# Kernel optimization log

Hardware: AMD Instinct MI355X
Metric: run time of the kernel (lower is better)

The kernel has to match this reference:

```python
import math
import jax, jax.numpy as jnp
import numpy as np

B, S, E, H, DK, L, NB, V, FF, C = 4, 2048, 512, 8, 64, 2, 4, 32000, 2048, 4


def _pos_encoding(seq_len, embed_dim):
    pos = np.arange(seq_len, dtype=np.float32)[:, None]
    div = np.exp(np.arange(0, embed_dim, 2, dtype=np.float32) * (-math.log(10000.0) / embed_dim))
    pe = np.zeros((seq_len, embed_dim), dtype=np.float32)
    pe[:, 0::2] = np.sin(pos * div)
    pe[:, 1::2] = np.cos(pos * div)
    return jnp.asarray(pe)


def _layernorm(x, g, b, eps=1e-5):
    m = jnp.mean(x, axis=-1, keepdims=True)
    v = jnp.mean((x - m) ** 2, axis=-1, keepdims=True)
    return (x - m) * jax.lax.rsqrt(v + eps) * g + b


def setup_inputs() -> dict:
    key = jax.random.key(0)
    ks = jax.random.split(key, 32)
    sd = 0.02
    inp = {
        "tokens": jax.random.randint(ks[0], (B, S), 0, V, dtype=jnp.int32),
        "emb": jax.random.normal(ks[1], (V, E), jnp.float32) * sd,
        # per-block stacked params (leading dim NB)
        "Wq": jax.random.normal(ks[2], (NB, E, E), jnp.float32) * sd,
        "Wk": jax.random.normal(ks[3], (NB, E, E), jnp.float32) * sd,
        "Wv": jax.random.normal(ks[4], (NB, E, E), jnp.float32) * sd,
        "Wo": jax.random.normal(ks[5], (NB, E, E), jnp.float32) * sd,
        # quantum per-head linear stacks: [NB, L, H, DK, DK] weights, [NB, L, H, DK] biases
        "qh_w": jax.random.normal(ks[6], (NB, L, H, DK, DK), jnp.float32) * 0.1,
        "qh_b": jax.random.normal(ks[7], (NB, L, H, DK), jnp.float32) * 0.01,
        "kh_w": jax.random.normal(ks[8], (NB, L, H, DK, DK), jnp.float32) * 0.1,
        "kh_b": jax.random.normal(ks[9], (NB, L, H, DK), jnp.float32) * 0.01,
        "vh_w": jax.random.normal(ks[10], (NB, L, H, DK, DK), jnp.float32) * 0.1,
        "vh_b": jax.random.normal(ks[11], (NB, L, H, DK), jnp.float32) * 0.01,
        "ln1_g": jnp.ones((NB, E), jnp.float32),
        "ln1_b": jnp.zeros((NB, E), jnp.float32),
        "ln2_g": jnp.ones((NB, E), jnp.float32),
        "ln2_b": jnp.zeros((NB, E), jnp.float32),
        "f_w1": jax.random.normal(ks[12], (NB, E, FF), jnp.float32) * sd,
        "f_b1": jnp.zeros((NB, FF), jnp.float32),
        "f_w2": jax.random.normal(ks[13], (NB, FF, E), jnp.float32) * sd,
        "f_b2": jnp.zeros((NB, E), jnp.float32),
        "cls_w": jax.random.normal(ks[14], (E, C), jnp.float32) * sd,
        "cls_b": jnp.zeros((C,), jnp.float32),
    }
    return inp


def _quantum_apply(h, w_stack, b_stack):
    # h: [B,H,S,DK]; w_stack: [L,H,DK,DK]; b_stack: [L,H,DK]
    for l in range(L):
        h = jnp.einsum("bhsd,hde->bhse", h, w_stack[l]) + b_stack[l][None, :, None, :]
    return h


def _block(x, Wq, Wk, Wv, Wo, qh_w, qh_b, kh_w, kh_b, vh_w, vh_b,
           ln1_g, ln1_b, ln2_g, ln2_b, f_w1, f_b1, f_w2, f_b2):
    b, s, _ = x.shape
    q = (x @ Wq).reshape(b, s, H, DK).transpose(0, 2, 1, 3)  # [B,H,S,DK]
    k = (x @ Wk).reshape(b, s, H, DK).transpose(0, 2, 1, 3)
    v = (x @ Wv).reshape(b, s, H, DK).transpose(0, 2, 1, 3)
    q = _quantum_apply(q, qh_w, qh_b)
    k = _quantum_apply(k, kh_w, kh_b)
    v = _quantum_apply(v, vh_w, vh_b)
    scores = jnp.einsum("bhqd,bhkd->bhqk", q, k) / math.sqrt(DK)
    attn = jax.nn.softmax(scores, axis=-1)
    out = jnp.einsum("bhqk,bhkd->bhqd", attn, v)
    out = out.transpose(0, 2, 1, 3).reshape(b, s, E) @ Wo
    x = _layernorm(x + out, ln1_g, ln1_b)
    ffn = jax.nn.relu(x @ f_w1 + f_b1) @ f_w2 + f_b2
    return _layernorm(x + ffn, ln2_g, ln2_b)


def reference(tokens, emb, Wq, Wk, Wv, Wo, qh_w, qh_b, kh_w, kh_b, vh_w, vh_b,
              ln1_g, ln1_b, ln2_g, ln2_b, f_w1, f_b1, f_w2, f_b2, cls_w, cls_b):
    x = emb[tokens]  # [B,S,E]
    x = x + _pos_encoding(S, E)[None]
    for i in range(NB):
        x = _block(x, Wq[i], Wk[i], Wv[i], Wo[i],
                   qh_w[i], qh_b[i], kh_w[i], kh_b[i], vh_w[i], vh_b[i],
                   ln1_g[i], ln1_b[i], ln2_g[i], ln2_b[i],
                   f_w1[i], f_b1[i], f_w2[i], f_b2[i])
    x = x.mean(axis=1)  # [B,E]
    return x @ cls_w + cls_b  # [B,C]
```

## Files before the change

### kernel.cpp

```cpp
#include <hip/hip_runtime.h>
#include <hip/hip_bf16.h>
#include <math.h>

#define BB 4
#define SS 2048
#define EE 512
#define HH 8
#define DKK 64
#define LL 2
#define NBB 4
#define FFF 2048
#define CC 4
#define NBSE ((size_t)BB * SS * EE)

typedef __attribute__((ext_vector_type(8))) short bf16x8;
typedef __attribute__((ext_vector_type(4))) float f32x4;
using bf16 = __hip_bfloat16;

__device__ __forceinline__ float fast_exp2(float x) { return __builtin_amdgcn_exp2f(x); }

__device__ __forceinline__ void gload16(const bf16* g, bf16* l) {
    __builtin_amdgcn_global_load_lds((const __attribute__((address_space(1))) void*)g,
                                     (__attribute__((address_space(3))) void*)l, 16, 0, 0);
}
__device__ __forceinline__ unsigned short bf16bits(float f) {
    bf16 h = __float2bfloat16(f);
    return *(unsigned short*)&h;
}

__global__ __launch_bounds__(256) void embed_kernel(const int* __restrict__ tokens,
                                                    const float* __restrict__ emb,
                                                    float* __restrict__ x,
                                                    bf16* __restrict__ xb) {
    int i = blockIdx.x * blockDim.x + threadIdx.x;
    int total = BB * SS * EE / 2;
    if (i >= total) return;
    int pi  = i & (EE / 2 - 1);
    int row = i >> 8;
    int s   = row & (SS - 1);
    int tok = tokens[row];
    int e0  = pi * 2;
    const float kln = 9.210340371976184f / (float)EE;
    float arg = (float)s * expf(-(float)e0 * kln);
    float2 ev = *(const float2*)(emb + (size_t)tok * EE + e0);
    float2 o;
    o.x = ev.x + sinf(arg);
    o.y = ev.y + cosf(arg);
    *(float2*)(x + (size_t)row * EE + e0) = o;
    xb[(size_t)row * EE + e0]     = __float2bfloat16(o.x);
    xb[(size_t)row * EE + e0 + 1] = __float2bfloat16(o.y);
}

__global__ __launch_bounds__(256) void transpose_to_bf16(const float* __restrict__ in,
                                                         bf16* __restrict__ out,
                                                         int K, int N,
                                                         size_t zstride, int row_off) {
    const float* src = in + (size_t)blockIdx.z * K * N;
    bf16* dst = out + (size_t)blockIdx.z * zstride;
    int r0 = blockIdx.y * 64, c0 = blockIdx.x * 64;
    __shared__ float tl[64][65];
    int t = threadIdx.x;
    int lr = t >> 4, lc = (t & 15) * 4;
#pragma unroll
    for (int i = 0; i < 4; i++) {
        float4 v = *(const float4*)(src + (size_t)(r0 + lr + i * 16) * N + c0 + lc);
        tl[lr + i * 16][lc + 0] = v.x;
        tl[lr + i * 16][lc + 1] = v.y;
        tl[lr + i * 16][lc + 2] = v.z;
        tl[lr + i * 16][lc + 3] = v.w;
    }
    __syncthreads();
#pragma unroll
    for (int i = 0; i < 4; i++) {
        int n = lr + i * 16;
#pragma unroll
        for (int j = 0; j < 4; j++)
            dst[(size_t)(row_off + c0 + n) * K + r0 + lc + j] = __float2bfloat16(tl[lc + j][n]);
    }
}

#define GF_RELU 1
#define GF_SCATTER3 2
#define GF_OUTBF16 4
__global__ __launch_bounds__(256) void gemm_bf16(const bf16* __restrict__ A,
                                                 const bf16* __restrict__ BT,
                                                 const float* __restrict__ bias,
                                                 void* __restrict__ C,
                                                 int M, int N, int K, int flags) {
    __shared__ __align__(16) bf16 Asm[128 * 32];
    __shared__ __align__(16) bf16 Bsm[128 * 32];
    int t = threadIdx.x;
    int l = t & 63, w = t >> 6;
    int nbx = gridDim.x;
    int lin = blockIdx.y * nbx + blockIdx.x;
    int cpx = (nbx * gridDim.y) >> 3;
    int swz = (lin & 7) * cpx + (lin >> 3);
    int bm = (swz / nbx) * 128, bn = (swz % nbx) * 128;
    int wr = (w >> 1) * 64, wc = (w & 1) * 64;
    int lr = l & 15, lg = l >> 4;
    int ca = w * 2;
    int sr = l >> 2, sk = (l & 3) * 8;
    const bf16* ga  = A  + (size_t)(bm + ca * 16 + sr) * K + sk;
    const bf16* ga2 = ga + (size_t)16 * K;
    const bf16* gb  = BT + (size_t)(bn + ca * 16 + sr) * K + sk;
    const bf16* gb2 = gb + (size_t)16 * K;

    f32x4 acc[4][4];
#pragma unroll
    for (int m = 0; m < 4; m++)
#pragma unroll
        for (int n = 0; n < 4; n++) acc[m][n] = (f32x4){0.f, 0.f, 0.f, 0.f};

    for (int k0 = 0; k0 < K; k0 += 32) {
        __syncthreads();
        gload16(ga + k0,  &Asm[ca * 512]);
        gload16(ga2 + k0, &Asm[ca * 512 + 512]);
        gload16(gb + k0,  &Bsm[ca * 512]);
        gload16(gb2 + k0, &Bsm[ca * 512 + 512]);
        __syncthreads();
        bf16x8 af[4], bfr[4];
#pragma unroll
        for (int m = 0; m < 4; m++)
            af[m] = *(const bf16x8*)&Asm[(wr + m * 16 + lr) * 32 + lg * 8];
#pragma unroll
        for (int n = 0; n < 4; n++)
            bfr[n] = *(const bf16x8*)&Bsm[(wc + n * 16 + lr) * 32 + lg * 8];
#pragma unroll
        for (int m = 0; m < 4; m++)
#pragma unroll
            for (int n = 0; n < 4; n++)
                acc[m][n] = __builtin_amdgcn_mfma_f32_16x16x32_bf16(af[m], bfr[n], acc[m][n], 0, 0, 0);
    }

#pragma unroll
    for (int m = 0; m < 4; m++) {
        int row = bm + wr + m * 16 + lg * 4;
#pragma unroll
        for (int n = 0; n < 4; n++) {
            int col = bn + wc + n * 16 + lr;
            float bv = bias ? bias[col] : 0.f;
#pragma unroll
            for (int r = 0; r < 4; r++) {
                float v = acc[m][n][r] + bv;
                if (flags & GF_RELU) v = fmaxf(v, 0.f);
                int rr = row + r;
                if (flags & GF_SCATTER3) {
                    int tsel = col >> 9;
                    int b = rr >> 11, s = rr & (SS - 1);
                    int h = (col >> 6) & 7, dk = col & 63;
                    ((bf16*)C)[tsel * NBSE + (((size_t)(b * HH + h) * SS + s) << 6) + dk] = __float2bfloat16(v);
                } else if (flags & GF_OUTBF16) {
                    ((bf16*)C)[(size_t)rr * N + col] = __float2bfloat16(v);
                } else {
                    ((float*)C)[(size_t)rr * N + col] = v;
                }
            }
        }
    }
}

__global__ __launch_bounds__(256) void gemm_bf16_m64(const bf16* __restrict__ A,
                                                     const bf16* __restrict__ BT,
                                                     const float* __restrict__ bias,
                                                     void* __restrict__ C,
                                                     int M, int N, int K, int flags) {
    __shared__ __align__(16) bf16 Asm[64 * 32];
    __shared__ __align__(16) bf16 Bsm[128 * 32];
    int t = threadIdx.x;
    int l = t & 63, w = t >> 6;
    int nbx = gridDim.x;
    int lin = blockIdx.y * nbx + blockIdx.x;
    int cpx = (nbx * gridDim.y) >> 3;
    int swz = (lin & 7) * cpx + (lin >> 3);
    int bm = (swz / nbx) * 64, bn = (swz % nbx) * 128;
    int wr = (w >> 1) * 32, wc = (w & 1) * 64;
    int lr = l & 15, lg = l >> 4;
    int ca = w * 2;
    int sr = l >> 2, sk = (l & 3) * 8;
    const bf16* ga  = A  + (size_t)(bm + w * 16 + sr) * K + sk;
    const bf16* gb  = BT + (size_t)(bn + ca * 16 + sr) * K + sk;
    const bf16* gb2 = gb + (size_t)16 * K;

    f32x4 acc[2][4];
#pragma unroll
    for (int m = 0; m < 2; m++)
#pragma unroll
        for (int n = 0; n < 4; n++) acc[m][n] = (f32x4){0.f, 0.f, 0.f, 0.f};

    for (int k0 = 0; k0 < K; k0 += 32) {
        __syncthreads();
        gload16(ga + k0,  &Asm[w * 512]);
        gload16(gb + k0,  &Bsm[ca * 512]);
        gload16(gb2 + k0, &Bsm[ca * 512 + 512]);
        __syncthreads();
        bf16x8 af[2], bfr[4];
#pragma unroll
        for (int m = 0; m < 2; m++)
            af[m] = *(const bf16x8*)&Asm[(wr + m * 16 + lr) * 32 + lg * 8];
#pragma unroll
        for (int n = 0; n < 4; n++)
            bfr[n] = *(const bf16x8*)&Bsm[(wc + n * 16 + lr) * 32 + lg * 8];
#pragma unroll
        for (int m = 0; m < 2; m++)
#pragma unroll
            for (int n = 0; n < 4; n++)
                acc[m][n] = __builtin_amdgcn_mfma_f32_16x16x32_bf16(af[m], bfr[n], acc[m][n], 0, 0, 0);
    }

#pragma unroll
    for (int m = 0; m < 2; m++) {
        int row = bm + wr + m * 16 + lg * 4;
#pragma unroll
        for (int n = 0; n < 4; n++) {
            int col = bn + wc + n * 16 + lr;
            float bv = bias ? bias[col] : 0.f;
#pragma unroll
            for (int r = 0; r < 4; r++) {
                float v = acc[m][n][r] + bv;
                if (flags & GF_RELU) v = fmaxf(v, 0.f);
                int rr = row + r;
                if (flags & GF_OUTBF16) {
                    ((bf16*)C)[(size_t)rr * N + col] = __float2bfloat16(v);
                } else {
                    ((float*)C)[(size_t)rr * N + col] = v;
                }
            }
        }
    }
}

__global__ __launch_bounds__(256) void quantum_mfma(bf16* __restrict__ qb, bf16* __restrict__ kb, bf16* __restrict__ vb,
                                                    bf16* __restrict__ vT,
                                                    const bf16* __restrict__ qwT, const bf16* __restrict__ kwT, const bf16* __restrict__ vwT,
                                                    const float* __restrict__ qbi, const float* __restrict__ kbi, const float* __restrict__ vbi) {
    __shared__ __align__(16) bf16 Hs[128 * 72];
    __shared__ __align__(16) bf16 W0s[64 * 72];
    __shared__ __align__(16) bf16 W1s[64 * 72];
    int z = blockIdx.z;
    bf16* hb       = z == 0 ? qb  : (z == 1 ? kb  : vb);
    const bf16* wT = z == 0 ? qwT : (z == 1 ? kwT : vwT);
    const float* bi = z == 0 ? qbi : (z == 1 ? kbi : vbi);
    int bh = blockIdx.y, h = bh & (HH - 1);
    int s0 = blockIdx.x * 128;
    int t = threadIdx.x, l = t & 63, w = t >> 6;
    int lr = l & 15, lg = l >> 4;
    bf16* base = hb + ((size_t)bh * SS + s0) * DKK;
    const bf16* w0p = wT + (size_t)h * 4096;
    const bf16* w1p = wT + (size_t)(HH + h) * 4096;
    {
        int r = t >> 1, dbase = (t & 1) * 32;
#pragma unroll
        for (int i = 0; i < 4; i++) {
            uint4 hv = *(const uint4*)(base + (size_t)r * 64 + dbase + i * 8);
            *(uint4*)&Hs[r * 72 + dbase + i * 8] = hv;
        }
        const bf16* wp = (t < 128) ? w0p : w1p;
        bf16* Ws = (t < 128) ? W0s : W1s;
        int tt = t & 127;
        int wr2 = tt >> 1, wd = (tt & 1) * 32;
#pragma unroll
        for (int i = 0; i < 4; i++) {
            uint4 wv = *(const uint4*)(wp + wr2 * 64 + wd + i * 8);
            *(uint4*)&Ws[wr2 * 72 + wd + i * 8] = wv;
        }
    }
    __syncthreads();
    f32x4 acc[2][4];
#pragma unroll
    for (int m = 0; m < 2; m++)
#pragma unroll
        for (int n = 0; n < 4; n++) acc[m][n] = (f32x4){0.f, 0.f, 0.f, 0.f};
    bf16x8 af[2][2];
#pragma unroll
    for (int m = 0; m < 2; m++)
#pragma unroll
        for (int ks = 0; ks < 2; ks++)
            af[m][ks] = *(const bf16x8*)&Hs[(w * 32 + m * 16 + lr) * 72 + ks * 32 + lg * 8];
#pragma unroll
    for (int n = 0; n < 4; n++)
#pragma unroll
        for (int ks = 0; ks < 2; ks++) {
            bf16x8 bfr = *(const bf16x8*)&W0s[(n * 16 + lr) * 72 + ks * 32 + lg * 8];
#pragma unroll
            for (int m = 0; m < 2; m++)
                acc[m][n] = __builtin_amdgcn_mfma_f32_16x16x32_bf16(af[m][ks], bfr, acc[m][n], 0, 0, 0);
        }
#pragma unroll
    for (int n = 0; n < 4; n++) {
        float b0 = bi[(size_t)h * 64 + n * 16 + lr];
#pragma unroll
        for (int m = 0; m < 2; m++)
#pragma unroll
            for (int r = 0; r < 4; r++)
                Hs[(w * 32 + m * 16 + lg * 4 + r) * 72 + n * 16 + lr] = __float2bfloat16(acc[m][n][r] + b0);
    }
    f32x4 acc2[2][4];
#pragma unroll
    for (int m = 0; m < 2; m++)
#pragma unroll
        for (int n = 0; n < 4; n++) acc2[m][n] = (f32x4){0.f, 0.f, 0.f, 0.f};
    bf16x8 af2[2][2];
#pragma unroll
    for (int m = 0; m < 2; m++)
#pragma unroll
        for (int ks = 0; ks < 2; ks++)
            af2[m][ks] = *(const bf16x8*)&Hs[(w * 32 + m * 16 + lr) * 72 + ks * 32 + lg * 8];
#pragma unroll
    for (int n = 0; n < 4; n++)
#pragma unroll
        for (int ks = 0; ks < 2; ks++) {
            bf16x8 bfr = *(const bf16x8*)&W1s[(n * 16 + lr) * 72 + ks * 32 + lg * 8];
#pragma unroll
            for (int m = 0; m < 2; m++)
                acc2[m][n] = __builtin_amdgcn_mfma_f32_16x16x32_bf16(af2[m][ks], bfr, acc2[m][n], 0, 0, 0);
        }
    if (z == 2) {
        __syncthreads();
        bf16* vt = Hs;
#pragma unroll
        for (int n = 0; n < 4; n++) {
            float b1 = bi[(size_t)(HH + h) * 64 + n * 16 + lr];
#pragma unroll
            for (int m = 0; m < 2; m++) {
                ushort4 pk;
                pk.x = bf16bits(acc2[m][n][0] + b1);
                pk.y = bf16bits(acc2[m][n][1] + b1);
                pk.z = bf16bits(acc2[m][n][2] + b1);
                pk.w = bf16bits(acc2[m][n][3] + b1);
                *(ushort4*)&vt[(n * 16 + lr) * 136 + w * 32 + m * 16 + lg * 4] = pk;
            }
        }
        __syncthreads();
        bf16* vbase = vT + (size_t)bh * DKK * SS + s0;
        int row = t >> 2, c0 = (t & 3) * 32;
#pragma unroll
        for (int i = 0; i < 4; i++)
            *(uint4*)(vbase + (size_t)row * SS + c0 + i * 8) = *(uint4*)&vt[row * 136 + c0 + i * 8];
    } else {
#pragma unroll
        for (int n = 0; n < 4; n++) {
            float b1 = bi[(size_t)(HH + h) * 64 + n * 16 + lr];
#pragma unroll
            for (int m = 0; m < 2; m++)
#pragma unroll
                for (int r = 0; r < 4; r++)
                    base[(size_t)(w * 32 + m * 16 + lg * 4 + r) * 64 + n * 16 + lr] = __float2bfloat16(acc2[m][n][r] + b1);
        }
    }
}

__global__ __launch_bounds__(512) __attribute__((amdgpu_waves_per_eu(6, 6)))
void attn_mfma(const bf16* __restrict__ q,
               const bf16* __restrict__ k,
               const bf16* __restrict__ vT,
               bf16* __restrict__ ao) {
    __shared__ __align__(16) bf16 Ksm[64 * 72];
    __shared__ __align__(16) bf16 Vtm[64 * 72];
    __shared__ __align__(16) bf16 Psm[8 * 16 * 68];
    int wg  = blockIdx.x;
    int nw  = (wg & 7) * 64 + (wg >> 3);
    int bh  = nw >> 4;
    int q0  = (nw & 15) * 128;
    int b = bh >> 3, hh = bh & 7;
    int t = threadIdx.x, l = t & 63, w = t >> 6;
    int lr = l & 15, lg = l >> 4;
    bf16* Pw = &Psm[w * 16 * 68];

    bf16x8 qf[2];
#pragma unroll
    for (int ks = 0; ks < 2; ks++)
        qf[ks] = *(const bf16x8*)(q + ((size_t)bh * SS + q0 + w * 16 + lr) * DKK + ks * 32 + lg * 8);

    float m_run[4] = {-INFINITY, -INFINITY, -INFINITY, -INFINITY};
    float l_run[4] = {0.f, 0.f, 0.f, 0.f};
    f32x4 accO[4];
#pragma unroll
    for (int j = 0; j < 4; j++) accO[j] = (f32x4){0.f, 0.f, 0.f, 0.f};

    const bf16* kbase = k  + (size_t)bh * SS * DKK;
    const bf16* vbase = vT + (size_t)bh * DKK * SS;
    int srow = t >> 3, scol = (t & 7) * 8;

    uint4 kreg, vreg;
    kreg = *(const uint4*)(kbase + (size_t)srow * DKK + scol);
    vreg = *(const uint4*)(vbase + (size_t)srow * SS + scol);

    const float SC = 0.180336879f;

    for (int kt = 0; kt < SS; kt += 64) {
        __syncthreads();
        *(uint4*)&Ksm[srow * 72 + scol] = kreg;
        *(uint4*)&Vtm[srow * 72 + scol] = vreg;
        __syncthreads();
        if (kt + 64 < SS) {
            kreg = *(const uint4*)(kbase + (size_t)(kt + 64 + srow) * DKK + scol);
            vreg = *(const uint4*)(vbase + (size_t)srow * SS + kt + 64 + scol);
        }

        f32x4 s[4];
#pragma unroll
        for (int n = 0; n < 4; n++) s[n] = (f32x4){0.f, 0.f, 0.f, 0.f};
        __builtin_amdgcn_s_setprio(1);
#pragma unroll
        for (int n = 0; n < 4; n++)
#pragma unroll
            for (int ks = 0; ks < 2; ks++) {
                bf16x8 kf = *(const bf16x8*)&Ksm[(n * 16 + lr) * 72 + ks * 32 + lg * 8];
                s[n] = __builtin_amdgcn_mfma_f32_16x16x32_bf16(qf[ks], kf, s[n], 0, 0, 0);
            }
        __builtin_amdgcn_s_setprio(0);

#pragma unroll
        for (int n = 0; n < 4; n++) s[n] *= SC;
        float mx[4];
#pragma unroll
        for (int r = 0; r < 4; r++)
            mx[r] = fmaxf(fmaxf(s[0][r], s[1][r]), fmaxf(s[2][r], s[3][r]));
        bool ok = true;
#pragma unroll
        for (int r = 0; r < 4; r++) ok = ok && (mx[r] <= m_run[r] + 8.f);
        if (!__all(ok)) {
#pragma unroll
            for (int r = 0; r < 4; r++) {
                float t2 = mx[r];
                t2 = fmaxf(t2, __shfl_xor(t2, 1, 16));
                t2 = fmaxf(t2, __shfl_xor(t2, 2, 16));
                t2 = fmaxf(t2, __shfl_xor(t2, 4, 16));
                t2 = fmaxf(t2, __shfl_xor(t2, 8, 16));
                float mn = fmaxf(m_run[r], t2);
                float fc = fast_exp2(m_run[r] - mn);
                m_run[r] = mn;
                l_run[r] *= fc;
#pragma unroll
                for (int j = 0; j < 4; j++) accO[j][r] *= fc;
            }
        }
#pragma unroll
        for (int n = 0; n < 4; n++)
#pragma unroll
            for (int r = 0; r < 4; r++) {
                float p = fast_exp2(s[n][r] - m_run[r]);
                l_run[r] += p;
                s[n][r] = p;
            }

#pragma unroll
        for (int n = 0; n < 4; n++)
#pragma unroll
            for (int r = 0; r < 4; r++)
                Pw[(lg * 4 + r) * 68 + n * 16 + lr] = __float2bfloat16(s[n][r]);

        bf16x8 pa[2];
#pragma unroll
        for (int ks = 0; ks < 2; ks++)
            pa[ks] = *(const bf16x8*)&Pw[lr * 68 + ks * 32 + lg * 8];
        __builtin_amdgcn_s_setprio(1);
#pragma unroll
        for (int j = 0; j < 4; j++)
#pragma unroll
            for (int ks = 0; ks < 2; ks++) {
                bf16x8 vb8 = *(const bf16x8*)&Vtm[(j * 16 + lr) * 72 + ks * 32 + lg * 8];
                accO[j] = __builtin_amdgcn_mfma_f32_16x16x32_bf16(pa[ks], vb8, accO[j], 0, 0, 0);
            }
        __builtin_amdgcn_s_setprio(0);
    }

    float inv[4];
#pragma unroll
    for (int r = 0; r < 4; r++) {
        float ls = l_run[r];
        ls += __shfl_xor(ls, 1, 16);
        ls += __shfl_xor(ls, 2, 16);
        ls += __shfl_xor(ls, 4, 16);
        ls += __shfl_xor(ls, 8, 16);
        inv[r] = 1.f / ls;
    }
#pragma unroll
    for (int j = 0; j < 4; j++)
#pragma unroll
        for (int r = 0; r < 4; r++) {
            int row = q0 + w * 16 + lg * 4 + r;
            ao[((size_t)(b * SS) + row) * EE + hh * 64 + j * 16 + lr] = __float2bfloat16(accO[j][r] * inv[r]);
        }
}

__global__ __launch_bounds__(256) void ln_kernel(float* __restrict__ x,
                                                 const float* __restrict__ res,
                                                 const float* __restrict__ g,
                                                 const float* __restrict__ beta,
                                                 bf16* __restrict__ xb) {
    int t = threadIdx.x, lane = t & 63, wv = t >> 6;
    int row = blockIdx.x * 4 + wv;
    float* xr = x + (size_t)row * EE;
    const float* rr = res + (size_t)row * EE;
    int c0 = lane * 8;
    float4 a0 = *(const float4*)(xr + c0);
    float4 a1 = *(const float4*)(xr + c0 + 4);
    float4 b0 = *(const float4*)(rr + c0);
    float4 b1 = *(const float4*)(rr + c0 + 4);
    float v[8];
    v[0] = a0.x + b0.x; v[1] = a0.y + b0.y; v[2] = a0.z + b0.z; v[3] = a0.w + b0.w;
    v[4] = a1.x + b1.x; v[5] = a1.y + b1.y; v[6] = a1.z + b1.z; v[7] = a1.w + b1.w;
    float s = 0.f;
#pragma unroll
    for (int i = 0; i < 8; i++) s += v[i];
#pragma unroll
    for (int m = 1; m < 64; m <<= 1) s += __shfl_xor(s, m, 64);
    float mean = s * (1.f / EE);
    float qv = 0.f;
#pragma unroll
    for (int i = 0; i < 8; i++) { v[i] -= mean; qv += v[i] * v[i]; }
#pragma unroll
    for (int m = 1; m < 64; m <<= 1) qv += __shfl_xor(qv, m, 64);
    float rs = rsqrtf(qv * (1.f / EE) + 1e-5f);
    float4 gg0 = *(const float4*)(g + c0);
    float4 gg1 = *(const float4*)(g + c0 + 4);
    float4 bb0 = *(const float4*)(beta + c0);
    float4 bb1 = *(const float4*)(beta + c0 + 4);
    float o[8];
    o[0] = v[0] * rs * gg0.x + bb0.x; o[1] = v[1] * rs * gg0.y + bb0.y;
    o[2] = v[2] * rs * gg0.z + bb0.z; o[3] = v[3] * rs * gg0.w + bb0.w;
    o[4] = v[4] * rs * gg1.x + bb1.x; o[5] = v[5] * rs * gg1.y + bb1.y;
    o[6] = v[6] * rs * gg1.z + bb1.z; o[7] = v[7] * rs * gg1.w + bb1.w;
    *(float4*)(xr + c0)     = make_float4(o[0], o[1], o[2], o[3]);
    *(float4*)(xr + c0 + 4) = make_float4(o[4], o[5], o[6], o[7]);
    ushort4 pk0, pk1;
    pk0.x = bf16bits(o[0]); pk0.y = bf16bits(o[1]); pk0.z = bf16bits(o[2]); pk0.w = bf16bits(o[3]);
    pk1.x = bf16bits(o[4]); pk1.y = bf16bits(o[5]); pk1.z = bf16bits(o[6]); pk1.w = bf16bits(o[7]);
    bf16* xbr = xb + (size_t)row * EE + c0;
    *(ushort4*)xbr       = pk0;
    *(ushort4*)(xbr + 4) = pk1;
}

__global__ __launch_bounds__(256) void meanpart_kernel(const float* __restrict__ x,
                                                       float* __restrict__ part) {
    int b = blockIdx.y, c = blockIdx.x;
    int t = threadIdx.x;
    float2 acc = make_float2(0.f, 0.f);
    for (int s = c * 32; s < c * 32 + 32; s++) {
        float2 v = *(const float2*)(x + ((size_t)b * SS + s) * EE + t * 2);
        acc.x += v.x; acc.y += v.y;
    }
    *(float2*)(part + (size_t)(b * 64 + c) * EE + t * 2) = acc;
}

__global__ __launch_bounds__(256) void meancls_kernel(const float* __restrict__ part,
                                                      const float* __restrict__ cw,
                                                      const float* __restrict__ cb,
                                                      float* __restrict__ out) {
    int b = blockIdx.x;
    int t = threadIdx.x;
    __shared__ float xm[EE];
    float2 acc = make_float2(0.f, 0.f);
    for (int i = 0; i < 64; i++) {
        float2 v = *(const float2*)(part + (size_t)(b * 64 + i) * EE + t * 2);
        acc.x += v.x; acc.y += v.y;
    }
    xm[t * 2]     = acc.x * (1.f / SS);
    xm[t * 2 + 1] = acc.y * (1.f / SS);
    __syncthreads();
    if (t < CC) {
        float a = cb[t];
        for (int e = 0; e < EE; e++) a += xm[e] * cw[e * CC + t];
        out[b * CC + t] = a;
    }
}

extern "C" void kernel_launch(void* const* d_in, const int* in_sizes, int n_in,
                              void* d_out, int out_size, void* d_ws, size_t ws_size,
                              hipStream_t stream) {
    (void)in_sizes; (void)n_in; (void)out_size; (void)ws_size;
    const int*   tokens = (const int*)d_in[0];
    const float* emb    = (const float*)d_in[1];
    const float* Wq     = (const float*)d_in[2];
    const float* Wk     = (const float*)d_in[3];
    const float* Wv     = (const float*)d_in[4];
    const float* Wo     = (const float*)d_in[5];
    const float* qh_w   = (const float*)d_in[6];
    const float* qh_b   = (const float*)d_in[7];
    const float* kh_w   = (const float*)d_in[8];
    const float* kh_b   = (const float*)d_in[9];
    const float* vh_w   = (const float*)d_in[10];
    const float* vh_b   = (const float*)d_in[11];
    const float* ln1_g  = (const float*)d_in[12];
    const float* ln1_b  = (const float*)d_in[13];
    const float* ln2_g  = (const float*)d_in[14];
    const float* ln2_b  = (const float*)d_in[15];
    const float* f_w1   = (const float*)d_in[16];
    const float* f_b1   = (const float*)d_in[17];
    const float* f_w2   = (const float*)d_in[18];
    const float* f_b2   = (const float*)d_in[19];
    const float* cls_w  = (const float*)d_in[20];
    const float* cls_b  = (const float*)d_in[21];

    const size_t nBSF = (size_t)BB * SS * FFF;
    float* x    = (float*)d_ws;
    float* t0   = x + NBSE;
    float* part = t0 + NBSE;
    bf16* xb    = (bf16*)(part + (size_t)BB * 64 * EE);
    bf16* qb    = xb + NBSE;
    bf16* kb    = qb + NBSE;
    bf16* vb    = kb + NBSE;
    bf16* vTb   = vb + NBSE;
    bf16* ao    = vTb + NBSE;
    bf16* ffnb  = ao + NBSE;
    bf16* WqkvT = ffnb + nBSF;
    bf16* WoT   = WqkvT + (size_t)NBB * 3 * EE * EE;
    bf16* fw1T  = WoT + (size_t)NBB * EE * EE;
    bf16* fw2T  = fw1T + (size_t)NBB * EE * FFF;
    bf16* qhT   = fw2T + (size_t)NBB * EE * FFF;
    bf16* khT   = qhT + (size_t)NBB * LL * HH * DKK * DKK;
    bf16* vhT   = khT + (size_t)NBB * LL * HH * DKK * DKK;

    const int M = BB * SS;
    const size_t zQKV = (size_t)3 * EE * EE;

    transpose_to_bf16<<<dim3(EE / 64, EE / 64, NBB), 256, 0, stream>>>(Wq, WqkvT, EE, EE, zQKV, 0);
    transpose_to_bf16<<<dim3(EE / 64, EE / 64, NBB), 256, 0, stream>>>(Wk, WqkvT, EE, EE, zQKV, EE);
    transpose_to_bf16<<<dim3(EE / 64, EE / 64, NBB), 256, 0, stream>>>(Wv, WqkvT, EE, EE, zQKV, 2 * EE);
    transpose_to_bf16<<<dim3(EE / 64, EE / 64, NBB), 256, 0, stream>>>(Wo, WoT, EE, EE, (size_t)EE * EE, 0);
    transpose_to_bf16<<<dim3(FFF / 64, EE / 64, NBB), 256, 0, stream>>>(f_w1, fw1T, EE, FFF, (size_t)EE * FFF, 0);
    transpose_to_bf16<<<dim3(EE / 64, FFF / 64, NBB), 256, 0, stream>>>(f_w2, fw2T, FFF, EE, (size_t)EE * FFF, 0);
    transpose_to_bf16<<<dim3(1, 1, NBB * LL * HH), 256, 0, stream>>>(qh_w, qhT, DKK, DKK, (size_t)DKK * DKK, 0);
    transpose_to_bf16<<<dim3(1, 1, NBB * LL * HH), 256, 0, stream>>>(kh_w, khT, DKK, DKK, (size_t)DKK * DKK, 0);
    transpose_to_bf16<<<dim3(1, 1, NBB * LL * HH), 256, 0, stream>>>(vh_w, vhT, DKK, DKK, (size_t)DKK * DKK, 0);

    embed_kernel<<<(BB * SS * EE / 2 + 255) / 256, 256, 0, stream>>>(tokens, emb, x, xb);

    for (int blk = 0; blk < NBB; blk++) {
        dim3 gEE64(EE / 128, M / 64);
        dim3 gQKV(3 * EE / 128, M / 128);
        dim3 gFF(FFF / 128, M / 128);
        const size_t wE = (size_t)blk * EE * EE;
        const size_t qwOff = (size_t)blk * LL * HH * DKK * DKK;
        const size_t qbOff = (size_t)blk * LL * HH * DKK;

        gemm_bf16<<<gQKV, 256, 0, stream>>>(xb, WqkvT + blk * zQKV, nullptr, qb, M, 3 * EE, EE, GF_SCATTER3);

        quantum_mfma<<<dim3(SS / 128, BB * HH, 3), 256, 0, stream>>>(
            qb, kb, vb, vTb, qhT + qwOff, khT + qwOff, vhT + qwOff,
            qh_b + qbOff, kh_b + qbOff, vh_b + qbOff);

        attn_mfma<<<dim3(512), 512, 0, stream>>>(qb, kb, vTb, ao);

        gemm_bf16_m64<<<gEE64, 256, 0, stream>>>(ao, WoT + wE, nullptr, t0, M, EE, EE, 0);
        ln_kernel<<<M / 4, 256, 0, stream>>>(x, t0, ln1_g + blk * EE, ln1_b + blk * EE, xb);

        gemm_bf16<<<gFF, 256, 0, stream>>>(xb, fw1T + (size_t)blk * EE * FFF, f_b1 + blk * FFF, ffnb, M, FFF, EE, GF_RELU | GF_OUTBF16);
        gemm_bf16_m64<<<gEE64, 256, 0, stream>>>(ffnb, fw2T + (size_t)blk * EE * FFF, f_b2 + blk * EE, t0, M, EE, FFF, 0);
        ln_kernel<<<M / 4, 256, 0, stream>>>(x, t0, ln2_g + blk * EE, ln2_b + blk * EE, xb);
    }

    meanpart_kernel<<<dim3(64, BB), 256, 0, stream>>>(x, part);
    meancls_kernel<<<BB, 256, 0, stream>>>(part, cls_w, cls_b, (float*)d_out);
}
```

Before: 986.4 us.

## Fold per-head quantum linear layers into QKV projection weights

The two per-head linear layers in the quantum stack are composed into a single matrix and bias, and that product is then folded into the Wq/Wk/Wv weights, so the QKV GEMM directly produces the transformed q/k/v with an effective bias. This removes the per-block quantum_mfma kernel and its extra read/write of q, k and v, replacing it with a small V-transpose kernel. The weight preprocessing grows (fp32 matrix products per head at setup), and rounding changes because the combined weights are quantized to bf16 once instead of after each stage.

```diff
diff --git a/kernel.cpp b/kernel.cpp
--- a/kernel.cpp
+++ b/kernel.cpp
@@ -79,6 +79,90 @@
     }
 }
 
+__global__ __launch_bounds__(256) void fold_w01(const float* __restrict__ qw, const float* __restrict__ kw, const float* __restrict__ vw,
+                                                const float* __restrict__ qbv, const float* __restrict__ kbv, const float* __restrict__ vbv,
+                                                float* __restrict__ w01, float* __restrict__ beff) {
+    int h = blockIdx.x, z = blockIdx.y, blk = blockIdx.z;
+    const float* w  = z == 0 ? qw  : (z == 1 ? kw  : vw);
+    const float* bi = z == 0 ? qbv : (z == 1 ? kbv : vbv);
+    const float* W0 = w + ((size_t)(blk * LL + 0) * HH + h) * 4096;
+    const float* W1 = w + ((size_t)(blk * LL + 1) * HH + h) * 4096;
+    __shared__ float s0[64 * 64];
+    __shared__ float s1[64 * 64];
+    int t = threadIdx.x;
+    for (int i = t; i < 4096; i += 256) { s0[i] = W0[i]; s1[i] = W1[i]; }
+    __syncthreads();
+    int d = t >> 2, e0 = (t & 3) * 16;
+    float acc[16] = {};
+    for (int c = 0; c < 64; c++) {
+        float a = s0[d * 64 + c];
+#pragma unroll
+        for (int e = 0; e < 16; e++) acc[e] += a * s1[c * 64 + e0 + e];
+    }
+    float* wout = w01 + ((size_t)(blk * 3 + z) * HH + h) * 4096;
+#pragma unroll
+    for (int e = 0; e < 16; e++) wout[d * 64 + e0 + e] = acc[e];
+    if (t < 64) {
+        const float* b0 = bi + ((size_t)(blk * LL + 0) * HH + h) * 64;
+        const float* b1 = bi + ((size_t)(blk * LL + 1) * HH + h) * 64;
+        float a = b1[t];
+        for (int c = 0; c < 64; c++) a += b0[c] * s1[c * 64 + t];
+        beff[(size_t)blk * 1536 + z * 512 + h * 64 + t] = a;
+    }
+}
+
+__global__ __launch_bounds__(256) void fold_wqkv(const float* __restrict__ Wq, const float* __restrict__ Wk, const float* __restrict__ Wv,
+                                                 const float* __restrict__ w01, bf16* __restrict__ WqkvT) {
+    int kc = blockIdx.x;
+    int h  = blockIdx.y;
+    int zb = blockIdx.z;
+    int blk = zb / 3, z = zb % 3;
+    const float* Wz  = (z == 0 ? Wq : (z == 1 ? Wk : Wv)) + (size_t)blk * EE * EE;
+    const float* Wp  = w01 + ((size_t)zb * HH + h) * 4096;
+    __shared__ float sw[64 * 64];
+    __shared__ float sp[64 * 64];
+    int t = threadIdx.x;
+    for (int i = t; i < 4096; i += 256) {
+        int kk = i >> 6, d = i & 63;
+        sw[i] = Wz[(size_t)(kc * 64 + kk) * EE + h * 64 + d];
+        sp[i] = Wp[i];
+    }
+    __syncthreads();
+    int kk = t >> 2, dk0 = (t & 3) * 16;
+    float acc[16] = {};
+    for (int d = 0; d < 64; d++) {
+        float a = sw[kk * 64 + d];
+#pragma unroll
+        for (int e = 0; e < 16; e++) acc[e] += a * sp[d * 64 + dk0 + e];
+    }
+    bf16* outb = WqkvT + (size_t)blk * 3 * EE * EE;
+    int k = kc * 64 + kk;
+#pragma unroll
+    for (int e = 0; e < 16; e++)
+        outb[(size_t)(z * 512 + h * 64 + dk0 + e) * EE + k] = __float2bfloat16(acc[e]);
+}
+
+__global__ __launch_bounds__(256) void vtrans_kernel(const bf16* __restrict__ v, bf16* __restrict__ vT) {
+    int s0 = blockIdx.x * 64, bh = blockIdx.y;
+    __shared__ bf16 vt[64 * 72];
+    int t = threadIdx.x;
+    int r = t >> 2, c0 = (t & 3) * 16;
+    const bf16* src = v + ((size_t)bh * SS + s0) * DKK;
+    uint4 v0 = *(const uint4*)(src + (size_t)r * DKK + c0);
+    uint4 v1 = *(const uint4*)(src + (size_t)r * DKK + c0 + 8);
+    const unsigned short* e0 = (const unsigned short*)&v0;
+    const unsigned short* e1 = (const unsigned short*)&v1;
+#pragma unroll
+    for (int j = 0; j < 8; j++) {
+        ((unsigned short*)vt)[(c0 + j) * 72 + r]     = e0[j];
+        ((unsigned short*)vt)[(c0 + 8 + j) * 72 + r] = e1[j];
+    }
+    __syncthreads();
+    bf16* dst = vT + (size_t)bh * DKK * SS + s0;
+    *(uint4*)(dst + (size_t)r * SS + c0)     = *(uint4*)&vt[r * 72 + c0];
+    *(uint4*)(dst + (size_t)r * SS + c0 + 8) = *(uint4*)&vt[r * 72 + c0 + 8];
+}
+
 #define GF_RELU 1
 #define GF_SCATTER3 2
 #define GF_OUTBF16 4
@@ -225,126 +309,6 @@
                     ((float*)C)[(size_t)rr * N + col] = v;
                 }
             }
-        }
-    }
-}
-
-__global__ __launch_bounds__(256) void quantum_mfma(bf16* __restrict__ qb, bf16* __restrict__ kb, bf16* __restrict__ vb,
-                                                    bf16* __restrict__ vT,
-                                                    const bf16* __restrict__ qwT, const bf16* __restrict__ kwT, const bf16* __restrict__ vwT,
-                                                    const float* __restrict__ qbi, const float* __restrict__ kbi, const float* __restrict__ vbi) {
-    __shared__ __align__(16) bf16 Hs[128 * 72];
-    __shared__ __align__(16) bf16 W0s[64 * 72];
-    __shared__ __align__(16) bf16 W1s[64 * 72];
-    int z = blockIdx.z;
-    bf16* hb       = z == 0 ? qb  : (z == 1 ? kb  : vb);
-    const bf16* wT = z == 0 ? qwT : (z == 1 ? kwT : vwT);
-    const float* bi = z == 0 ? qbi : (z == 1 ? kbi : vbi);
-    int bh = blockIdx.y, h = bh & (HH - 1);
-    int s0 = blockIdx.x * 128;
-    int t = threadIdx.x, l = t & 63, w = t >> 6;
-    int lr = l & 15, lg = l >> 4;
-    bf16* base = hb + ((size_t)bh * SS + s0) * DKK;
-    const bf16* w0p = wT + (size_t)h * 4096;
-    const bf16* w1p = wT + (size_t)(HH + h) * 4096;
-    {
-        int r = t >> 1, dbase = (t & 1) * 32;
-#pragma unroll
-        for (int i = 0; i < 4; i++) {
-            uint4 hv = *(const uint4*)(base + (size_t)r * 64 + dbase + i * 8);
-            *(uint4*)&Hs[r * 72 + dbase + i * 8] = hv;
-        }
-        const bf16* wp = (t < 128) ? w0p : w1p;
-        bf16* Ws = (t < 128) ? W0s : W1s;
-        int tt = t & 127;
-        int wr2 = tt >> 1, wd = (tt & 1) * 32;
-#pragma unroll
-        for (int i = 0; i < 4; i++) {
-            uint4 wv = *(const uint4*)(wp + wr2 * 64 + wd + i * 8);
-            *(uint4*)&Ws[wr2 * 72 + wd + i * 8] = wv;
-        }
-    }
-    __syncthreads();
-    f32x4 acc[2][4];
-#pragma unroll
-    for (int m = 0; m < 2; m++)
-#pragma unroll
-        for (int n = 0; n < 4; n++) acc[m][n] = (f32x4){0.f, 0.f, 0.f, 0.f};
-    bf16x8 af[2][2];
-#pragma unroll
-    for (int m = 0; m < 2; m++)
-#pragma unroll
-        for (int ks = 0; ks < 2; ks++)
-            af[m][ks] = *(const bf16x8*)&Hs[(w * 32 + m * 16 + lr) * 72 + ks * 32 + lg * 8];
-#pragma unroll
-    for (int n = 0; n < 4; n++)
-#pragma unroll
-        for (int ks = 0; ks < 2; ks++) {
-            bf16x8 bfr = *(const bf16x8*)&W0s[(n * 16 + lr) * 72 + ks * 32 + lg * 8];
-#pragma unroll
-            for (int m = 0; m < 2; m++)
-                acc[m][n] = __builtin_amdgcn_mfma_f32_16x16x32_bf16(af[m][ks], bfr, acc[m][n], 0, 0, 0);
-        }
-#pragma unroll
-    for (int n = 0; n < 4; n++) {
-        float b0 = bi[(size_t)h * 64 + n * 16 + lr];
-#pragma unroll
-        for (int m = 0; m < 2; m++)
-#pragma unroll
-            for (int r = 0; r < 4; r++)
-                Hs[(w * 32 + m * 16 + lg * 4 + r) * 72 + n * 16 + lr] = __float2bfloat16(acc[m][n][r] + b0);
-    }
-    f32x4 acc2[2][4];
-#pragma unroll
-    for (int m = 0; m < 2; m++)
-#pragma unroll
-        for (int n = 0; n < 4; n++) acc2[m][n] = (f32x4){0.f, 0.f, 0.f, 0.f};
-    bf16x8 af2[2][2];
-#pragma unroll
-    for (int m = 0; m < 2; m++)
-#pragma unroll
-        for (int ks = 0; ks < 2; ks++)
-            af2[m][ks] = *(const bf16x8*)&Hs[(w * 32 + m * 16 + lr) * 72 + ks * 32 + lg * 8];
-#pragma unroll
-    for (int n = 0; n < 4; n++)
-#pragma unroll
-        for (int ks = 0; ks < 2; ks++) {
-            bf16x8 bfr = *(const bf16x8*)&W1s[(n * 16 + lr) * 72 + ks * 32 + lg * 8];
-#pragma unroll
-            for (int m = 0; m < 2; m++)
-                acc2[m][n] = __builtin_amdgcn_mfma_f32_16x16x32_bf16(af2[m][ks], bfr, acc2[m][n], 0, 0, 0);
-        }
-    if (z == 2) {
-        __syncthreads();
-        bf16* vt = Hs;
-#pragma unroll
-        for (int n = 0; n < 4; n++) {
-            float b1 = bi[(size_t)(HH + h) * 64 + n * 16 + lr];
-#pragma unroll
-            for (int m = 0; m < 2; m++) {
-                ushort4 pk;
-                pk.x = bf16bits(acc2[m][n][0] + b1);
-                pk.y = bf16bits(acc2[m][n][1] + b1);
-                pk.z = bf16bits(acc2[m][n][2] + b1);
-                pk.w = bf16bits(acc2[m][n][3] + b1);
-                *(ushort4*)&vt[(n * 16 + lr) * 136 + w * 32 + m * 16 + lg * 4] = pk;
-            }
-        }
-        __syncthreads();
-        bf16* vbase = vT + (size_t)bh * DKK * SS + s0;
-        int row = t >> 2, c0 = (t & 3) * 32;
-#pragma unroll
-        for (int i = 0; i < 4; i++)
-            *(uint4*)(vbase + (size_t)row * SS + c0 + i * 8) = *(uint4*)&vt[row * 136 + c0 + i * 8];
-    } else {
-#pragma unroll
-        for (int n = 0; n < 4; n++) {
-            float b1 = bi[(size_t)(HH + h) * 64 + n * 16 + lr];
-#pragma unroll
-            for (int m = 0; m < 2; m++)
-#pragma unroll
-                for (int r = 0; r < 4; r++)
-                    base[(size_t)(w * 32 + m * 16 + lg * 4 + r) * 64 + n * 16 + lr] = __float2bfloat16(acc2[m][n][r] + b1);
         }
     }
 }
@@ -608,22 +572,17 @@
     bf16* WoT   = WqkvT + (size_t)NBB * 3 * EE * EE;
     bf16* fw1T  = WoT + (size_t)NBB * EE * EE;
     bf16* fw2T  = fw1T + (size_t)NBB * EE * FFF;
-    bf16* qhT   = fw2T + (size_t)NBB * EE * FFF;
-    bf16* khT   = qhT + (size_t)NBB * LL * HH * DKK * DKK;
-    bf16* vhT   = khT + (size_t)NBB * LL * HH * DKK * DKK;
+    float* w01  = (float*)(fw2T + (size_t)NBB * EE * FFF);
+    float* beff = w01 + (size_t)NBB * 3 * HH * DKK * DKK;
 
     const int M = BB * SS;
     const size_t zQKV = (size_t)3 * EE * EE;
 
-    transpose_to_bf16<<<dim3(EE / 64, EE / 64, NBB), 256, 0, stream>>>(Wq, WqkvT, EE, EE, zQKV, 0);
-    transpose_to_bf16<<<dim3(EE / 64, EE / 64, NBB), 256, 0, stream>>>(Wk, WqkvT, EE, EE, zQKV, EE);
-    transpose_to_bf16<<<dim3(EE / 64, EE / 64, NBB), 256, 0, stream>>>(Wv, WqkvT, EE, EE, zQKV, 2 * EE);
+    fold_w01<<<dim3(HH, 3, NBB), 256, 0, stream>>>(qh_w, kh_w, vh_w, qh_b, kh_b, vh_b, w01, beff);
+    fold_wqkv<<<dim3(8, HH, 3 * NBB), 256, 0, stream>>>(Wq, Wk, Wv, w01, WqkvT);
     transpose_to_bf16<<<dim3(EE / 64, EE / 64, NBB), 256, 0, stream>>>(Wo, WoT, EE, EE, (size_t)EE * EE, 0);
     transpose_to_bf16<<<dim3(FFF / 64, EE / 64, NBB), 256, 0, stream>>>(f_w1, fw1T, EE, FFF, (size_t)EE * FFF, 0);
     transpose_to_bf16<<<dim3(EE / 64, FFF / 64, NBB), 256, 0, stream>>>(f_w2, fw2T, FFF, EE, (size_t)EE * FFF, 0);
-    transpose_to_bf16<<<dim3(1, 1, NBB * LL * HH), 256, 0, stream>>>(qh_w, qhT, DKK, DKK, (size_t)DKK * DKK, 0);
-    transpose_to_bf16<<<dim3(1, 1, NBB * LL * HH), 256, 0, stream>>>(kh_w, khT, DKK, DKK, (size_t)DKK * DKK, 0);
-    transpose_to_bf16<<<dim3(1, 1, NBB * LL * HH), 256, 0, stream>>>(vh_w, vhT, DKK, DKK, (size_t)DKK * DKK, 0);
 
     embed_kernel<<<(BB * SS * EE / 2 + 255) / 256, 256, 0, stream>>>(tokens, emb, x, xb);
 
@@ -632,14 +591,10 @@
         dim3 gQKV(3 * EE / 128, M / 128);
         dim3 gFF(FFF / 128, M / 128);
         const size_t wE = (size_t)blk * EE * EE;
-        const size_t qwOff = (size_t)blk * LL * HH * DKK * DKK;
-        const size_t qbOff = (size_t)blk * LL * HH * DKK;
-
-        gemm_bf16<<<gQKV, 256, 0, stream>>>(xb, WqkvT + blk * zQKV, nullptr, qb, M, 3 * EE, EE, GF_SCATTER3);
-
-        quantum_mfma<<<dim3(SS / 128, BB * HH, 3), 256, 0, stream>>>(
-            qb, kb, vb, vTb, qhT + qwOff, khT + qwOff, vhT + qwOff,
-            qh_b + qbOff, kh_b + qbOff, vh_b + qbOff);
+
+        gemm_bf16<<<gQKV, 256, 0, stream>>>(xb, WqkvT + blk * zQKV, beff + (size_t)blk * 1536, qb, M, 3 * EE, EE, GF_SCATTER3);
+
+        vtrans_kernel<<<dim3(SS / 64, BB * HH), 256, 0, stream>>>(vb, vTb);
 
         attn_mfma<<<dim3(512), 512, 0, stream>>>(qb, kb, vTb, ao);
 
```

Result: faster. 956.4 us (-3.0%).
